# Optimization experiments

Hardware: AMD Instinct MI355X
Metric: run time of the kernel (lower is better)

Reference implementation:

```python
import jax, jax.numpy as jnp
import numpy as np

B, C, H, W = 64, 3, 512, 512
MAX_HOLES = 5
MAX_LEN = 170  # int(H * 1/3), exclusive upper bound for hole side length


def setup_inputs() -> dict:
    key = jax.random.key(0)
    k_img, k_n, k_y, k_x, k_h, k_w = jax.random.split(key, 6)
    return {
        "img": jax.random.normal(k_img, (B, C, H, W), dtype=jnp.float32),
        "num_holes": jax.random.randint(k_n, (B,), 0, MAX_HOLES, dtype=jnp.int32),
        "ys": jax.random.randint(k_y, (B, MAX_HOLES), 0, H, dtype=jnp.int32),
        "xs": jax.random.randint(k_x, (B, MAX_HOLES), 0, W, dtype=jnp.int32),
        "hs": jax.random.randint(k_h, (B, MAX_HOLES), 1, MAX_LEN, dtype=jnp.int32),
        "ws": jax.random.randint(k_w, (B, MAX_HOLES), 1, MAX_LEN, dtype=jnp.int32),
    }


def reference(img, num_holes, ys, xs, hs, ws):
    b, c, h, w = img.shape
    k = ys.shape[1]
    # Box edges, clamped to image bounds (matches torch clamp semantics).
    y1 = jnp.clip(ys - hs // 2, 0, h)[:, :, None]  # [B,K,1]
    y2 = jnp.clip(ys + hs // 2, 0, h)[:, :, None]
    x1 = jnp.clip(xs - ws // 2, 0, w)[:, :, None]
    x2 = jnp.clip(xs + ws // 2, 0, w)[:, :, None]
    rows = jnp.arange(h)[None, None, :]  # [1,1,H]
    cols = jnp.arange(w)[None, None, :]  # [1,1,W]
    in_y = (rows >= y1) & (rows < y2)  # [B,K,H]
    in_x = (cols >= x1) & (cols < x2)  # [B,K,W]
    # Only the first num_holes[i] boxes are active for sample i.
    active = (jnp.arange(k)[None, :] < num_holes[:, None])  # [B,K]
    inside = (in_y[:, :, :, None] & in_x[:, :, None, :]) & active[:, :, None, None]  # [B,K,H,W]
    mask = ~jnp.any(inside, axis=1)  # [B,H,W] True = keep pixel
    return img * mask[:, None, :, :].astype(img.dtype)
```

## Files before the change

### kernel.cpp

```cpp
#include <hip/hip_runtime.h>


#define BB 64
#define CC 3
#define HH 512
#define WW 512
#define KK 5
#define W4 (WW / 4)
#define PLANE4 (HH * W4)

typedef float v4f __attribute__((ext_vector_type(4)));

__global__ __launch_bounds__(256) void cutout_kernel(
    const v4f* __restrict__ img,
    const int* __restrict__ num_holes,
    const int* __restrict__ ys,
    const int* __restrict__ xs,
    const int* __restrict__ hs,
    const int* __restrict__ ws,
    v4f* __restrict__ out)
{
    int plane = blockIdx.y;
    int b     = plane / 3;
    int pos   = blockIdx.x * 256 + threadIdx.x;
    int y     = pos >> 7;
    int x0    = (pos & 127) << 2;

    float m0 = 1.0f, m1 = 1.0f, m2 = 1.0f, m3 = 1.0f;

    int n = num_holes[b];
    for (int k = 0; k < n; ++k) {
        int yc = ys[b * KK + k];
        int xc = xs[b * KK + k];
        int hh = hs[b * KK + k];
        int wv = ws[b * KK + k];
        int y1 = max(0, yc - hh / 2);
        int y2 = min(HH, yc + hh / 2);
        int x1 = max(0, xc - wv / 2);
        int x2 = min(WW, xc + wv / 2);
        bool iny = (y >= y1) & (y < y2);
        if (iny) {
            if ((x0 + 0) >= x1 && (x0 + 0) < x2) m0 = 0.0f;
            if ((x0 + 1) >= x1 && (x0 + 1) < x2) m1 = 0.0f;
            if ((x0 + 2) >= x1 && (x0 + 2) < x2) m2 = 0.0f;
            if ((x0 + 3) >= x1 && (x0 + 3) < x2) m3 = 0.0f;
        }
    }

    size_t q = (size_t)plane * PLANE4 + (size_t)pos;
    v4f v = img[q];
    v.x *= m0; v.y *= m1; v.z *= m2; v.w *= m3;
    out[q] = v;
}

extern "C" void kernel_launch(void* const* d_in, const int* in_sizes, int n_in,
                              void* d_out, int out_size, void* d_ws, size_t ws_size,
                              hipStream_t stream) {
    const v4f* img         = (const v4f*)d_in[0];
    const int* num_holes   = (const int*)d_in[1];
    const int* ys          = (const int*)d_in[2];
    const int* xs          = (const int*)d_in[3];
    const int* hs          = (const int*)d_in[4];
    const int* ws          = (const int*)d_in[5];
    v4f* out               = (v4f*)d_out;

    dim3 grid(PLANE4 / 256, BB * CC);
    cutout_kernel<<<grid, dim3(256), 0, stream>>>(img, num_holes, ys, xs, hs, ws, out);
}
```

Baseline: 73.07 us.

## Process multiple float4 chunks per thread with hoisted hole bounds

Each thread now handles eight float4 elements strided across the plane instead of one, shrinking the grid eightfold. All loads are issued up front to increase memory-level parallelism. The per-sample hole bounds are computed once per thread with a fully unrolled loop, and inactive holes are disabled by zeroing their y-end. The trade-off is higher register use per thread and fewer blocks, which can lower occupancy for a purely bandwidth-bound copy.

```diff
diff --git a/kernel.cpp b/kernel.cpp
--- a/kernel.cpp
+++ b/kernel.cpp
@@ -8,6 +8,8 @@
 #define KK 5
 #define W4 (WW / 4)
 #define PLANE4 (HH * W4)
+#define TPP 8192
+#define ITER (PLANE4 / TPP)
 
 typedef float v4f __attribute__((ext_vector_type(4)));
 
@@ -22,35 +24,48 @@
 {
     int plane = blockIdx.y;
     int b     = plane / 3;
-    int pos   = blockIdx.x * 256 + threadIdx.x;
-    int y     = pos >> 7;
-    int x0    = (pos & 127) << 2;
-
-    float m0 = 1.0f, m1 = 1.0f, m2 = 1.0f, m3 = 1.0f;
+    int tid   = blockIdx.x * 256 + threadIdx.x;
 
     int n = num_holes[b];
-    for (int k = 0; k < n; ++k) {
+    int sy1[KK], sy2[KK], sx1[KK], sx2[KK];
+#pragma unroll
+    for (int k = 0; k < KK; ++k) {
         int yc = ys[b * KK + k];
         int xc = xs[b * KK + k];
         int hh = hs[b * KK + k];
         int wv = ws[b * KK + k];
-        int y1 = max(0, yc - hh / 2);
-        int y2 = min(HH, yc + hh / 2);
-        int x1 = max(0, xc - wv / 2);
-        int x2 = min(WW, xc + wv / 2);
-        bool iny = (y >= y1) & (y < y2);
-        if (iny) {
-            if ((x0 + 0) >= x1 && (x0 + 0) < x2) m0 = 0.0f;
-            if ((x0 + 1) >= x1 && (x0 + 1) < x2) m1 = 0.0f;
-            if ((x0 + 2) >= x1 && (x0 + 2) < x2) m2 = 0.0f;
-            if ((x0 + 3) >= x1 && (x0 + 3) < x2) m3 = 0.0f;
-        }
+        sy1[k] = max(0, yc - hh / 2);
+        sy2[k] = (k < n) ? min(HH, yc + hh / 2) : 0;
+        sx1[k] = max(0, xc - wv / 2);
+        sx2[k] = min(WW, xc + wv / 2);
     }
 
-    size_t q = (size_t)plane * PLANE4 + (size_t)pos;
-    v4f v = img[q];
-    v.x *= m0; v.y *= m1; v.z *= m2; v.w *= m3;
-    out[q] = v;
+    size_t qbase = (size_t)plane * PLANE4 + (size_t)tid;
+
+    v4f v[ITER];
+#pragma unroll
+    for (int i = 0; i < ITER; ++i)
+        v[i] = img[qbase + (size_t)(i * TPP)];
+
+#pragma unroll
+    for (int i = 0; i < ITER; ++i) {
+        int pos = tid + i * TPP;
+        int y   = pos >> 7;
+        int x0  = (pos & 127) << 2;
+        float m0 = 1.0f, m1 = 1.0f, m2 = 1.0f, m3 = 1.0f;
+#pragma unroll
+        for (int k = 0; k < KK; ++k) {
+            if (y >= sy1[k] && y < sy2[k]) {
+                if ((x0 + 0) >= sx1[k] && (x0 + 0) < sx2[k]) m0 = 0.0f;
+                if ((x0 + 1) >= sx1[k] && (x0 + 1) < sx2[k]) m1 = 0.0f;
+                if ((x0 + 2) >= sx1[k] && (x0 + 2) < sx2[k]) m2 = 0.0f;
+                if ((x0 + 3) >= sx1[k] && (x0 + 3) < sx2[k]) m3 = 0.0f;
+            }
+        }
+        v4f t = v[i];
+        t.x *= m0; t.y *= m1; t.z *= m2; t.w *= m3;
+        out[qbase + (size_t)(i * TPP)] = t;
+    }
 }
 
 extern "C" void kernel_launch(void* const* d_in, const int* in_sizes, int n_in,
@@ -64,6 +79,6 @@
     const int* ws          = (const int*)d_in[5];
     v4f* out               = (v4f*)d_out;
 
-    dim3 grid(PLANE4 / 256, BB * CC);
+    dim3 grid(TPP / 256, BB * CC);
     cutout_kernel<<<grid, dim3(256), 0, stream>>>(img, num_holes, ys, xs, hs, ws, out);
 }
```

Result: slower. 77.21 us (+5.7%).
